# Kernel tuning notes

Measured on AMD Instinct MI355X. Metric: run time of the kernel, lower is better.

The kernel has to match this reference:

```python
import jax, jax.numpy as jnp
import numpy as np
from jax import lax

EMB_DIM = 16
NUM_EMB = 32
DN = ('NCDHW', 'OIDHW', 'NCDHW')


def conv3d(x, w, b, stride, pad):
    y = lax.conv_general_dilated(x, w, window_strides=(stride,) * 3,
                                 padding=[(pad, pad)] * 3, dimension_numbers=DN)
    return y + b[None, :, None, None, None]


def deconv3d(x, w, b, stride, pad):
    # PyTorch ConvTranspose3d: weight (Cin,Cout,k,k,k); equivalent to conv with
    # spatially flipped, channel-transposed kernel, lhs_dilation=stride, pad=k-1-p.
    k = w.shape[-1]
    wf = jnp.flip(w, axis=(2, 3, 4)).transpose(1, 0, 2, 3, 4)  # (Cout,Cin,k,k,k)
    y = lax.conv_general_dilated(x, wf, window_strides=(1, 1, 1),
                                 padding=[(k - 1 - pad, k - 1 - pad)] * 3,
                                 lhs_dilation=(stride,) * 3, dimension_numbers=DN)
    return y + b[None, :, None, None, None]


def setup_inputs() -> dict:
    key = jax.random.key(0)
    ks = jax.random.split(key, 16)
    x = jax.random.normal(ks[0], (16, 3, 16, 128, 128), dtype=jnp.float32)
    s = 0.05
    # encoder params
    enc_w1 = jax.random.normal(ks[1], (4, 3, 4, 4, 4), jnp.float32) * s
    enc_b1 = jnp.zeros((4,), jnp.float32)
    enc_w2 = jax.random.normal(ks[2], (8, 4, 4, 4, 4), jnp.float32) * s
    enc_b2 = jnp.zeros((8,), jnp.float32)
    enc_w4 = jax.random.normal(ks[3], (EMB_DIM, 8, 3, 3, 3), jnp.float32) * s
    enc_b4 = jnp.zeros((EMB_DIM,), jnp.float32)
    # decoder params (ConvTranspose3d layout: (Cin, Cout, k, k, k))
    dec_w1 = jax.random.normal(ks[4], (EMB_DIM, 8, 4, 4, 4), jnp.float32) * s
    dec_b1 = jnp.zeros((8,), jnp.float32)
    dec_w3 = jax.random.normal(ks[5], (8, 4, 4, 4, 4), jnp.float32) * s
    dec_b3 = jnp.zeros((4,), jnp.float32)
    dec_w4 = jax.random.normal(ks[6], (4, 3, 3, 3, 3), jnp.float32) * s
    dec_b4 = jnp.zeros((3,), jnp.float32)
    # codebook buffers: normalize(randn)*0.1, rows 0/1 forced
    e = jax.random.normal(ks[7], (NUM_EMB, EMB_DIM), jnp.float32)
    e = e / jnp.linalg.norm(e, axis=1, keepdims=True) * 0.1
    embedding = e.at[0].set(0.0).at[1].set(6.0)
    cluster_size = jnp.ones((NUM_EMB,), jnp.float32)
    return dict(x=x, epoch=60,
                enc_w1=enc_w1, enc_b1=enc_b1, enc_w2=enc_w2, enc_b2=enc_b2,
                enc_w4=enc_w4, enc_b4=enc_b4,
                dec_w1=dec_w1, dec_b1=dec_b1, dec_w3=dec_w3, dec_b3=dec_b3,
                dec_w4=dec_w4, dec_b4=dec_b4,
                embedding=embedding, cluster_size=cluster_size)


def reference(x, epoch, enc_w1, enc_b1, enc_w2, enc_b2, enc_w4, enc_b4,
              dec_w1, dec_b1, dec_w3, dec_b3, dec_w4, dec_b4,
              embedding, cluster_size):
    # ---- Encoder ----
    h = jax.nn.relu(conv3d(x, enc_w1, enc_b1, 2, 1))
    h = jax.nn.relu(conv3d(h, enc_w2, enc_b2, 2, 1))
    z = jnp.clip(conv3d(h, enc_w4, enc_b4, 1, 1), 0.0, 6.0)  # relu(relu6(.))
    B, C, Dd, Hh, Ww = z.shape

    # ---- VQ-EMA forward (epoch >= 50 branch) ----
    emb = embedding.at[0].set(0.0).at[1].set(6.0)
    flat = z.transpose(0, 2, 3, 4, 1).reshape(-1, C)  # (N, D)
    # squared euclidean distances; argmin matches cdist argmin
    d2 = (jnp.sum(flat * flat, axis=1, keepdims=True)
          - 2.0 * flat @ emb.T + jnp.sum(emb * emb, axis=1))
    idx = jnp.argmin(d2, axis=1)                       # (N,)
    q = emb[idx]                                       # (N, D)
    quant = q.reshape(B, Dd, Hh, Ww, C).transpose(0, 4, 1, 2, 3)

    N = flat.shape[0]
    avg_probs = jnp.zeros((NUM_EMB,), flat.dtype).at[idx].add(1.0) / N
    perplexity = jnp.exp(-jnp.sum(avg_probs * jnp.log(avg_probs + 1e-10)))
    used_codes = jnp.sum(cluster_size > 1e-5).astype(jnp.float32) / NUM_EMB

    quantized_st = z + lax.stop_gradient(quant - z)
    vq_loss = 0.25 * jnp.mean((lax.stop_gradient(quant) - z) ** 2)
    codes = idx.reshape(B, Dd, Hh, Ww)

    # ---- Decoder ----
    d = jax.nn.relu(deconv3d(quantized_st, dec_w1, dec_b1, 2, 1))
    d = jax.nn.relu(deconv3d(d, dec_w3, dec_b3, 2, 1))
    out = deconv3d(d, dec_w4, dec_b4, 1, 1)
    return out, vq_loss, codes, perplexity, used_codes
```

## Files before the change

### kernel.cpp

```cpp
#include <hip/hip_runtime.h>
#include <math.h>

#define NB 16


__device__ __forceinline__ float4 ld4(const float* p) {
  return *reinterpret_cast<const float4*>(p);
}
__device__ __forceinline__ void st4(float* p, float4 v) {
  *reinterpret_cast<float4*>(p) = v;
}

__global__ __launch_bounds__(256) void conv1_k(
    const float* __restrict__ x, const float* __restrict__ w,
    const float* __restrict__ bias, float* __restrict__ y) {
  int idx = blockIdx.x * 256 + threadIdx.x;
  int g  = idx & 15;
  int oh = (idx >> 4) & 63;
  int od = (idx >> 10) & 7;
  int n  = idx >> 13;
  bool gl = (g > 0), gr = (g < 15);
  float acc[4][4];
  #pragma unroll
  for (int co = 0; co < 4; co++) {
    float bv = bias[co];
    #pragma unroll
    for (int m = 0; m < 4; m++) acc[co][m] = bv;
  }
  int ih0 = 2 * oh - 1;
  #pragma unroll 1
  for (int ci = 0; ci < 3; ci++) {
    #pragma unroll 1
    for (int kd = 0; kd < 4; kd++) {
      int id = 2 * od - 1 + kd;
      bool vd = (unsigned)id < 16u;
      int idc = vd ? id : 0;
      const float* plane = x + (((n * 3 + ci) * 16 + idc) * 16384);
      #pragma unroll
      for (int kh = 0; kh < 4; kh++) {
        int ih = ih0 + kh;
        bool v = vd && ((unsigned)ih < 128u);
        int ihc = (unsigned)ih < 128u ? ih : 0;
        const float* rp = plane + ihc * 128 + 8 * g;
        float r[10];
        float4 A = ld4(rp);
        float4 B = ld4(rp + 4);
        float rl = rp[-1 * (int)gl];
        float rr = rp[gr ? 8 : 0];
        r[0] = (v && gl) ? rl : 0.0f;
        r[1] = v ? A.x : 0.0f; r[2] = v ? A.y : 0.0f;
        r[3] = v ? A.z : 0.0f; r[4] = v ? A.w : 0.0f;
        r[5] = v ? B.x : 0.0f; r[6] = v ? B.y : 0.0f;
        r[7] = v ? B.z : 0.0f; r[8] = v ? B.w : 0.0f;
        r[9] = (v && gr) ? rr : 0.0f;
        #pragma unroll
        for (int co = 0; co < 4; co++) {
          const float* wb = w + ((co * 3 + ci) * 4 + kd) * 16 + kh * 4;
          #pragma unroll
          for (int kw = 0; kw < 4; kw++) {
            float wv = wb[kw];
            #pragma unroll
            for (int m = 0; m < 4; m++)
              acc[co][m] += r[2 * m + kw] * wv;
          }
        }
      }
    }
  }
  #pragma unroll
  for (int co = 0; co < 4; co++) {
    float4 o;
    o.x = fmaxf(acc[co][0], 0.0f); o.y = fmaxf(acc[co][1], 0.0f);
    o.z = fmaxf(acc[co][2], 0.0f); o.w = fmaxf(acc[co][3], 0.0f);
    st4(y + ((n * 4 + co) * 8 + od) * 4096 + oh * 64 + 4 * g, o);
  }
}

__global__ __launch_bounds__(256) void conv2_k(
    const float* __restrict__ y1, const float* __restrict__ w,
    const float* __restrict__ bias, float* __restrict__ y) {
  int idx = blockIdx.x * 256 + threadIdx.x;
  int ow = idx & 31;
  int oh = (idx >> 5) & 31;
  int od = (idx >> 10) & 3;
  int n = (idx >> 12) & 15;
  int cog = idx >> 16;
  float acc[4];
  #pragma unroll
  for (int co = 0; co < 4; co++) acc[co] = bias[cog * 4 + co];
  int id0 = 2 * od - 1, ih0 = 2 * oh - 1, iw0 = 2 * ow - 1;
  bool vh[4], vw[4];
  #pragma unroll
  for (int l = 0; l < 4; l++) {
    vh[l] = (unsigned)(ih0 + l) < 64u;
    vw[l] = (unsigned)(iw0 + l) < 64u;
  }
  #pragma unroll 1
  for (int ci = 0; ci < 4; ci++) {
    const float* ip = y1 + ((n * 4 + ci) * 8) * 4096;
    #pragma unroll
    for (int kd = 0; kd < 4; kd++) {
      int id = id0 + kd;
      bool vd = (unsigned)id < 8u;
      const float* pp = ip + id * 4096;
      float p[4][4];
      #pragma unroll
      for (int kh = 0; kh < 4; kh++)
        #pragma unroll
        for (int kw = 0; kw < 4; kw++)
          p[kh][kw] = (vd && vh[kh] && vw[kw]) ? pp[(ih0 + kh) * 64 + (iw0 + kw)] : 0.0f;
      #pragma unroll
      for (int co = 0; co < 4; co++) {
        const float* wp = w + (((cog * 4 + co) * 4 + ci) * 4 + kd) * 16;
        #pragma unroll
        for (int kh = 0; kh < 4; kh++)
          #pragma unroll
          for (int kw = 0; kw < 4; kw++)
            acc[co] += p[kh][kw] * wp[kh * 4 + kw];
      }
    }
  }
  #pragma unroll
  for (int co = 0; co < 4; co++)
    y[((n * 8 + cog * 4 + co) * 4 + od) * 1024 + oh * 32 + ow] = fmaxf(acc[co], 0.0f);
}

__global__ __launch_bounds__(256) void conv4vq_k(
    const float* __restrict__ y2, const float* __restrict__ w,
    const float* __restrict__ bias, const float* __restrict__ emb,
    float* __restrict__ quant, float* __restrict__ codes_out,
    float* __restrict__ stats) {
  __shared__ float se[32 * 16];
  __shared__ float se2[32];
  __shared__ float shist[32];
  __shared__ float swred[4];
  int tid = threadIdx.x;
  for (int i = tid; i < 512; i += 256) {
    int r = i >> 4;
    float v = emb[i];
    if (r == 0) v = 0.0f;
    else if (r == 1) v = 6.0f;
    se[i] = v;
  }
  if (tid < 32) shist[tid] = 0.0f;
  __syncthreads();
  if (tid < 32) {
    float s = 0.0f;
    #pragma unroll
    for (int d = 0; d < 16; d++) { float v = se[tid * 16 + d]; s += v * v; }
    se2[tid] = s;
  }
  __syncthreads();

  int idx = blockIdx.x * 256 + tid;
  int ow = idx & 31;
  int oh = (idx >> 5) & 31;
  int od = (idx >> 10) & 3;
  int n  = idx >> 12;

  float acc[16];
  #pragma unroll
  for (int co = 0; co < 16; co++) acc[co] = bias[co];
  bool vh[3], vw[3];
  #pragma unroll
  for (int l = 0; l < 3; l++) {
    vh[l] = (unsigned)(oh - 1 + l) < 32u;
    vw[l] = (unsigned)(ow - 1 + l) < 32u;
  }
  #pragma unroll 1
  for (int ci = 0; ci < 8; ci++) {
    const float* ip = y2 + ((n * 8 + ci) * 4) * 1024;
    #pragma unroll
    for (int kd = 0; kd < 3; kd++) {
      int id = od - 1 + kd;
      bool vd = (unsigned)id < 4u;
      const float* pp = ip + id * 1024;
      float p[3][3];
      #pragma unroll
      for (int kh = 0; kh < 3; kh++)
        #pragma unroll
        for (int kw = 0; kw < 3; kw++)
          p[kh][kw] = (vd && vh[kh] && vw[kw]) ? pp[(oh - 1 + kh) * 32 + (ow - 1 + kw)] : 0.0f;
      #pragma unroll
      for (int co = 0; co < 16; co++) {
        const float* wp = w + ((co * 8 + ci) * 3 + kd) * 9;
        #pragma unroll
        for (int kh = 0; kh < 3; kh++)
          #pragma unroll
          for (int kw = 0; kw < 3; kw++)
            acc[co] += p[kh][kw] * wp[kh * 3 + kw];
      }
    }
  }
  float f2 = 0.0f;
  #pragma unroll
  for (int c = 0; c < 16; c++) {
    float v = fminf(fmaxf(acc[c], 0.0f), 6.0f);
    acc[c] = v;
    f2 += v * v;
  }

  float lsum = 0.0f;
  {
    float best = 1e30f; int bi = 0;
    for (int e = 0; e < 32; e++) {
      float dot = 0.0f;
      #pragma unroll
      for (int c = 0; c < 16; c++) dot += acc[c] * se[e * 16 + c];
      float d2 = f2 - 2.0f * dot + se2[e];
      if (d2 < best) { best = d2; bi = e; }
    }
    float* qp = quant + n * 65536 + od * 1024 + oh * 32 + ow;
    #pragma unroll
    for (int c = 0; c < 16; c++) {
      float q = se[bi * 16 + c];
      qp[c * 4096] = q;
      float df = q - acc[c];
      lsum += df * df;
    }
    codes_out[idx] = (float)bi;
    atomicAdd(&shist[bi], 1.0f);
  }
  for (int o = 32; o; o >>= 1) lsum += __shfl_down(lsum, o);
  if ((tid & 63) == 0) swred[tid >> 6] = lsum;
  __syncthreads();
  if (tid == 0) atomicAdd(&stats[0], swred[0] + swred[1] + swred[2] + swred[3]);
  if (tid < 32) {
    float h = shist[tid];
    if (h != 0.0f) atomicAdd(&stats[1 + tid], h);
  }
}

__global__ void init_stats_k(float* __restrict__ stats) {
  int tid = threadIdx.x;
  if (tid < 33) stats[tid] = 0.0f;
}

__global__ void fin_k(const float* __restrict__ stats,
                      const float* __restrict__ cluster_size,
                      float* __restrict__ out_loss, float* __restrict__ out_perp,
                      float* __restrict__ out_used) {
  int tid = threadIdx.x;
  float v = 0.0f;
  float used = 0.0f;
  if (tid < 32) {
    float p = stats[1 + tid] * (1.0f / 65536.0f);
    v = p * logf(p + 1e-10f);
    used = (cluster_size[tid] > 1e-5f) ? 1.0f : 0.0f;
  }
  for (int o = 16; o; o >>= 1) { v += __shfl_down(v, o); used += __shfl_down(used, o); }
  if (tid == 0) {
    *out_perp = expf(-v);
    *out_used = used * (1.0f / 32.0f);
    *out_loss = 0.25f * stats[0] * (1.0f / 1048576.0f);
  }
}

__global__ __launch_bounds__(256) void deconv1_k(
    const float* __restrict__ q, const float* __restrict__ w,
    const float* __restrict__ bias, float* __restrict__ d1) {
  int bid = blockIdx.x;
  int cog = bid & 1;
  int ph  = (bid >> 1) & 1;
  int od  = (bid >> 2) & 7;
  int n   = bid >> 5;
  int tid = threadIdx.x;
  int g   = tid & 7;
  int bl  = tid >> 3;
  bool glf = (g > 0), grf = (g < 7);

  int kd0 = (od + 1) & 1;
  int idtop = (od + 1 - kd0) >> 1;
  int kh0 = (ph + 1) & 1;
  int ihtop = bl + ph;

  float acc[4][8];
  #pragma unroll
  for (int co = 0; co < 4; co++) {
    float bv = bias[cog * 4 + co];
    #pragma unroll
    for (int m = 0; m < 8; m++) acc[co][m] = bv;
  }

  #pragma unroll 1
  for (int ci = 0; ci < 16; ci++) {
    const float* ip = q + ((n * 16 + ci) * 4) * 1024;
    #pragma unroll
    for (int jd = 0; jd < 2; jd++) {
      int id = idtop - jd;
      bool vd = (unsigned)id < 4u;
      int idc = vd ? id : 0;
      const float* plane = ip + idc * 1024;
      #pragma unroll
      for (int jh = 0; jh < 2; jh++) {
        int ih = ihtop - jh;
        bool v = vd && ((unsigned)ih < 32u);
        int ihc = (unsigned)ih < 32u ? ih : 0;
        const float* rp = plane + ihc * 32 + 4 * g;
        float r[6];
        float4 A = ld4(rp);
        float rl = rp[-1 * (int)glf];
        float rr = rp[grf ? 4 : 0];
        r[0] = (v && glf) ? rl : 0.0f;
        r[1] = v ? A.x : 0.0f; r[2] = v ? A.y : 0.0f;
        r[3] = v ? A.z : 0.0f; r[4] = v ? A.w : 0.0f;
        r[5] = (v && grf) ? rr : 0.0f;
        int kd = kd0 + 2 * jd;
        int kh = kh0 + 2 * jh;
        #pragma unroll
        for (int co = 0; co < 4; co++) {
          const float* wb = w + ((ci * 8 + cog * 4 + co) * 4 + kd) * 16 + kh * 4;
          #pragma unroll
          for (int jw = 0; jw < 2; jw++) {
            float w_ev = wb[1 + 2 * jw];
            float w_od = wb[2 * jw];
            #pragma unroll
            for (int ii = 0; ii < 4; ii++) {
              acc[co][2 * ii]     += r[ii + 1 - jw] * w_ev;
              acc[co][2 * ii + 1] += r[ii + 2 - jw] * w_od;
            }
          }
        }
      }
    }
  }
  int oh = 2 * bl + ph;
  #pragma unroll
  for (int co = 0; co < 4; co++) {
    float* op = d1 + ((n * 8 + cog * 4 + co) * 8 + od) * 4096 + oh * 64 + 8 * g;
    float4 lo, hi;
    lo.x = fmaxf(acc[co][0], 0.0f); lo.y = fmaxf(acc[co][1], 0.0f);
    lo.z = fmaxf(acc[co][2], 0.0f); lo.w = fmaxf(acc[co][3], 0.0f);
    hi.x = fmaxf(acc[co][4], 0.0f); hi.y = fmaxf(acc[co][5], 0.0f);
    hi.z = fmaxf(acc[co][6], 0.0f); hi.w = fmaxf(acc[co][7], 0.0f);
    st4(op, lo); st4(op + 4, hi);
  }
}

__global__ __launch_bounds__(256) void deconv3_k(
    const float* __restrict__ d1, const float* __restrict__ w,
    const float* __restrict__ bias, float* __restrict__ d2) {
  int bid = blockIdx.x;
  int ph  = bid & 1;
  int blh = (bid >> 1) & 3;
  int od  = (bid >> 3) & 15;
  int n   = bid >> 7;
  int tid = threadIdx.x;
  int g   = tid & 15;
  int bl  = tid >> 4;
  int BL  = blh * 16 + bl;
  bool glf = (g > 0), grf = (g < 15);

  int kd0 = (od + 1) & 1;
  int idtop = (od + 1 - kd0) >> 1;
  int kh0 = (ph + 1) & 1;
  int ihtop = BL + ph;

  float acc[4][8];
  #pragma unroll
  for (int co = 0; co < 4; co++) {
    float bv = bias[co];
    #pragma unroll
    for (int m = 0; m < 8; m++) acc[co][m] = bv;
  }

  #pragma unroll 1
  for (int ci = 0; ci < 8; ci++) {
    const float* ip = d1 + ((n * 8 + ci) * 8) * 4096;
    #pragma unroll
    for (int jd = 0; jd < 2; jd++) {
      int id = idtop - jd;
      bool vd = (unsigned)id < 8u;
      int idc = vd ? id : 0;
      const float* plane = ip + idc * 4096;
      #pragma unroll
      for (int jh = 0; jh < 2; jh++) {
        int ih = ihtop - jh;
        bool v = vd && ((unsigned)ih < 64u);
        int ihc = (unsigned)ih < 64u ? ih : 0;
        const float* rp = plane + ihc * 64 + 4 * g;
        float r[6];
        float4 A = ld4(rp);
        float rl = rp[-1 * (int)glf];
        float rr = rp[grf ? 4 : 0];
        r[0] = (v && glf) ? rl : 0.0f;
        r[1] = v ? A.x : 0.0f; r[2] = v ? A.y : 0.0f;
        r[3] = v ? A.z : 0.0f; r[4] = v ? A.w : 0.0f;
        r[5] = (v && grf) ? rr : 0.0f;
        int kd = kd0 + 2 * jd;
        int kh = kh0 + 2 * jh;
        #pragma unroll
        for (int co = 0; co < 4; co++) {
          const float* wb = w + ((ci * 4 + co) * 4 + kd) * 16 + kh * 4;
          #pragma unroll
          for (int jw = 0; jw < 2; jw++) {
            float w_ev = wb[1 + 2 * jw];
            float w_od = wb[2 * jw];
            #pragma unroll
            for (int ii = 0; ii < 4; ii++) {
              acc[co][2 * ii]     += r[ii + 1 - jw] * w_ev;
              acc[co][2 * ii + 1] += r[ii + 2 - jw] * w_od;
            }
          }
        }
      }
    }
  }
  int oh = 2 * BL + ph;
  #pragma unroll
  for (int co = 0; co < 4; co++) {
    float* op = d2 + ((n * 4 + co) * 16 + od) * 16384 + oh * 128 + 8 * g;
    float4 lo, hi;
    lo.x = fmaxf(acc[co][0], 0.0f); lo.y = fmaxf(acc[co][1], 0.0f);
    lo.z = fmaxf(acc[co][2], 0.0f); lo.w = fmaxf(acc[co][3], 0.0f);
    hi.x = fmaxf(acc[co][4], 0.0f); hi.y = fmaxf(acc[co][5], 0.0f);
    hi.z = fmaxf(acc[co][6], 0.0f); hi.w = fmaxf(acc[co][7], 0.0f);
    st4(op, lo); st4(op + 4, hi);
  }
}

__global__ __launch_bounds__(256) void deconv4_k(
    const float* __restrict__ d2, const float* __restrict__ w,
    const float* __restrict__ bias, float* __restrict__ out) {
  int idx = blockIdx.x * 256 + threadIdx.x;
  int c = idx & 63;
  int b = (idx >> 6) & 63;
  int a = (idx >> 12) & 7;
  int n = idx >> 15;
  float acc[2][2][2][3];
  #pragma unroll
  for (int pd = 0; pd < 2; pd++)
    #pragma unroll
    for (int ph = 0; ph < 2; ph++)
      #pragma unroll
      for (int pw = 0; pw < 2; pw++)
        #pragma unroll
        for (int co = 0; co < 3; co++) acc[pd][ph][pw][co] = bias[co];
  int ih0 = 2 * b - 1, iw0 = 2 * c - 1;
  bool vh[4], vw[4];
  #pragma unroll
  for (int l = 0; l < 4; l++) {
    vh[l] = (unsigned)(ih0 + l) < 128u;
    vw[l] = (unsigned)(iw0 + l) < 128u;
  }
  #pragma unroll 1
  for (int ci = 0; ci < 4; ci++) {
    const float* ip = d2 + ((n * 4 + ci) * 16) * 16384;
    #pragma unroll
    for (int ld = 0; ld < 4; ld++) {
      int id = 2 * a - 1 + ld;
      bool vdl = (unsigned)id < 16u;
      const float* pp = ip + id * 16384;
      float p[4][4];
      #pragma unroll
      for (int lh = 0; lh < 4; lh++)
        #pragma unroll
        for (int lw = 0; lw < 4; lw++)
          p[lh][lw] = (vdl && vh[lh] && vw[lw]) ? pp[(ih0 + lh) * 128 + (iw0 + lw)] : 0.0f;
      #pragma unroll
      for (int pd = 0; pd < 2; pd++) {
        int kd = pd + 2 - ld;
        if (kd < 0 || kd > 2) continue;
        #pragma unroll
        for (int kh = 0; kh < 3; kh++)
          #pragma unroll
          for (int kw = 0; kw < 3; kw++)
            #pragma unroll
            for (int co = 0; co < 3; co++) {
              float wv = w[(ci * 3 + co) * 27 + kd * 9 + kh * 3 + kw];
              #pragma unroll
              for (int ph = 0; ph < 2; ph++)
                #pragma unroll
                for (int pw = 0; pw < 2; pw++)
                  acc[pd][ph][pw][co] += p[ph + 2 - kh][pw + 2 - kw] * wv;
            }
      }
    }
  }
  #pragma unroll
  for (int co = 0; co < 3; co++)
    #pragma unroll
    for (int pd = 0; pd < 2; pd++)
      #pragma unroll
      for (int ph = 0; ph < 2; ph++)
        #pragma unroll
        for (int pw = 0; pw < 2; pw++)
          out[((n * 3 + co) * 16 + 2 * a + pd) * 16384 +
              (2 * b + ph) * 128 + (2 * c + pw)] = acc[pd][ph][pw][co];
}

extern "C" void kernel_launch(void* const* d_in, const int* in_sizes, int n_in,
                              void* d_out, int out_size, void* d_ws, size_t ws_size,
                              hipStream_t stream) {
  const float* x      = (const float*)d_in[0];
  const float* enc_w1 = (const float*)d_in[2];
  const float* enc_b1 = (const float*)d_in[3];
  const float* enc_w2 = (const float*)d_in[4];
  const float* enc_b2 = (const float*)d_in[5];
  const float* enc_w4 = (const float*)d_in[6];
  const float* enc_b4 = (const float*)d_in[7];
  const float* dec_w1 = (const float*)d_in[8];
  const float* dec_b1 = (const float*)d_in[9];
  const float* dec_w3 = (const float*)d_in[10];
  const float* dec_b3 = (const float*)d_in[11];
  const float* dec_w4 = (const float*)d_in[12];
  const float* dec_b4 = (const float*)d_in[13];
  const float* emb    = (const float*)d_in[14];
  const float* csize  = (const float*)d_in[15];

  float* ws = (float*)d_ws;
  float* stats = ws;
  float* quant = ws + 64;
  float* y2    = ws + 64 + 2 * 1048576;
  float* y1    = y2 + 524288;
  float* d1    = ws + 64 + 1048576;
  float* d2    = ws + 64 + 1048576 + 4194304;

  float* out   = (float*)d_out;
  float* out_loss  = out + 12582912;
  float* out_codes = out_loss + 1;
  float* out_perp  = out_codes + 65536;
  float* out_used  = out_perp + 1;

  init_stats_k<<<1, 64, 0, stream>>>(stats);

  conv1_k<<<512, 256, 0, stream>>>(x, enc_w1, enc_b1, y1);
  conv2_k<<<512, 256, 0, stream>>>(y1, enc_w2, enc_b2, y2);

  conv4vq_k<<<256, 256, 0, stream>>>(y2, enc_w4, enc_b4, emb, quant, out_codes, stats);
  fin_k<<<1, 64, 0, stream>>>(stats, csize, out_loss, out_perp, out_used);

  deconv1_k<<<512, 256, 0, stream>>>(quant, dec_w1, dec_b1, d1);
  deconv3_k<<<2048, 256, 0, stream>>>(d1, dec_w3, dec_b3, d2);
  deconv4_k<<<2048, 256, 0, stream>>>(d2, dec_w4, dec_b4, out);
}
```

Before: 402.7 us.

## Split conv4+VQ output channels across thread groups to raise block count

The fused conv4/VQ kernel now gives each block 64 spatial positions, with four 64-thread groups each computing four of the sixteen output channels, so the launch grows from 256 to 1024 blocks. Conv results are staged in a padded shared tile, and a single wavefront then does the codebook argmin, writes, histogram and loss reduction. The aim is more parallelism and lower register pressure in the convolution part. In exchange, the VQ phase runs on only one wave per block, and input patches are reloaded by each channel group.

```diff
diff --git a/kernel.cpp b/kernel.cpp
--- a/kernel.cpp
+++ b/kernel.cpp
@@ -133,7 +133,7 @@
   __shared__ float se[32 * 16];
   __shared__ float se2[32];
   __shared__ float shist[32];
-  __shared__ float swred[4];
+  __shared__ float zsh[64][17];
   int tid = threadIdx.x;
   for (int i = tid; i < 512; i += 256) {
     int r = i >> 4;
@@ -150,17 +150,19 @@
     for (int d = 0; d < 16; d++) { float v = se[tid * 16 + d]; s += v * v; }
     se2[tid] = s;
   }
-  __syncthreads();
-
-  int idx = blockIdx.x * 256 + tid;
-  int ow = idx & 31;
-  int oh = (idx >> 5) & 31;
-  int od = (idx >> 10) & 3;
-  int n  = idx >> 12;
-
-  float acc[16];
-  #pragma unroll
-  for (int co = 0; co < 16; co++) acc[co] = bias[co];
+
+  int bid = blockIdx.x;
+  int ohg = bid & 15;
+  int od  = (bid >> 4) & 3;
+  int n   = bid >> 6;
+  int pos = tid & 63;
+  int cog = tid >> 6;
+  int ow  = pos & 31;
+  int oh  = ohg * 2 + (pos >> 5);
+
+  float acc[4];
+  #pragma unroll
+  for (int co = 0; co < 4; co++) acc[co] = bias[cog * 4 + co];
   bool vh[3], vw[3];
   #pragma unroll
   for (int l = 0; l < 3; l++) {
@@ -182,8 +184,8 @@
         for (int kw = 0; kw < 3; kw++)
           p[kh][kw] = (vd && vh[kh] && vw[kw]) ? pp[(oh - 1 + kh) * 32 + (ow - 1 + kw)] : 0.0f;
       #pragma unroll
-      for (int co = 0; co < 16; co++) {
-        const float* wp = w + ((co * 8 + ci) * 3 + kd) * 9;
+      for (int co = 0; co < 4; co++) {
+        const float* wp = w + (((cog * 4 + co) * 8 + ci) * 3 + kd) * 9;
         #pragma unroll
         for (int kh = 0; kh < 3; kh++)
           #pragma unroll
@@ -192,39 +194,41 @@
       }
     }
   }
-  float f2 = 0.0f;
-  #pragma unroll
-  for (int c = 0; c < 16; c++) {
-    float v = fminf(fmaxf(acc[c], 0.0f), 6.0f);
-    acc[c] = v;
-    f2 += v * v;
-  }
-
-  float lsum = 0.0f;
-  {
+  #pragma unroll
+  for (int co = 0; co < 4; co++)
+    zsh[pos][cog * 4 + co] = fminf(fmaxf(acc[co], 0.0f), 6.0f);
+  __syncthreads();
+
+  if (tid < 64) {
+    float f[16];
+    float f2 = 0.0f;
+    #pragma unroll
+    for (int c = 0; c < 16; c++) { float v = zsh[tid][c]; f[c] = v; f2 += v * v; }
     float best = 1e30f; int bi = 0;
     for (int e = 0; e < 32; e++) {
       float dot = 0.0f;
       #pragma unroll
-      for (int c = 0; c < 16; c++) dot += acc[c] * se[e * 16 + c];
+      for (int c = 0; c < 16; c++) dot += f[c] * se[e * 16 + c];
       float d2 = f2 - 2.0f * dot + se2[e];
       if (d2 < best) { best = d2; bi = e; }
     }
-    float* qp = quant + n * 65536 + od * 1024 + oh * 32 + ow;
+    int poh = ohg * 2 + (tid >> 5);
+    int pow_ = tid & 31;
+    float* qp = quant + n * 65536 + od * 1024 + poh * 32 + pow_;
+    float lsum = 0.0f;
     #pragma unroll
     for (int c = 0; c < 16; c++) {
       float q = se[bi * 16 + c];
       qp[c * 4096] = q;
-      float df = q - acc[c];
+      float df = q - f[c];
       lsum += df * df;
     }
-    codes_out[idx] = (float)bi;
+    codes_out[n * 4096 + od * 1024 + poh * 32 + pow_] = (float)bi;
     atomicAdd(&shist[bi], 1.0f);
-  }
-  for (int o = 32; o; o >>= 1) lsum += __shfl_down(lsum, o);
-  if ((tid & 63) == 0) swred[tid >> 6] = lsum;
+    for (int o = 32; o; o >>= 1) lsum += __shfl_down(lsum, o);
+    if (tid == 0) atomicAdd(&stats[0], lsum);
+  }
   __syncthreads();
-  if (tid == 0) atomicAdd(&stats[0], swred[0] + swred[1] + swred[2] + swred[3]);
   if (tid < 32) {
     float h = shist[tid];
     if (h != 0.0f) atomicAdd(&stats[1 + tid], h);
@@ -527,7 +531,7 @@
   conv1_k<<<512, 256, 0, stream>>>(x, enc_w1, enc_b1, y1);
   conv2_k<<<512, 256, 0, stream>>>(y1, enc_w2, enc_b2, y2);
 
-  conv4vq_k<<<256, 256, 0, stream>>>(y2, enc_w4, enc_b4, emb, quant, out_codes, stats);
+  conv4vq_k<<<1024, 256, 0, stream>>>(y2, enc_w4, enc_b4, emb, quant, out_codes, stats);
   fin_k<<<1, 64, 0, stream>>>(stats, csize, out_loss, out_perp, out_used);
 
   deconv1_k<<<512, 256, 0, stream>>>(quant, dec_w1, dec_b1, d1);
```

New measurement: 379.0 us. -5.9%, faster.
